# Performance work log

Hardware: AMD Instinct MI355X
Metric: run time of the kernel (lower is better)

Reference implementation:

```python
import jax, jax.numpy as jnp
import numpy as np


def setup_inputs() -> dict:
    key = jax.random.key(0)
    k1, k2, k3 = jax.random.split(key, 3)
    inp = jax.random.normal(k1, (32, 128, 56, 56), dtype=jnp.float32)
    # kaiming-style scale for a 3x3 conv kernel
    fan_in = 128 * 3 * 3
    kernel = jax.random.normal(k2, (256, 128, 3, 3), dtype=jnp.float32) * np.float32(np.sqrt(2.0 / fan_in))
    bias = jax.random.normal(k3, (256,), dtype=jnp.float32)
    return {"inp": inp, "kernel": kernel, "bias": bias}


def reference(inp, kernel, bias):
    # 3x3 conv, stride 1, padding 1 (SAME), NCHW / OIHW layout, plus bias.
    out = jax.lax.conv_general_dilated(
        inp, kernel,
        window_strides=(1, 1),
        padding=((1, 1), (1, 1)),
        dimension_numbers=("NCHW", "OIHW", "NCHW"),
    )
    return out + bias[None, :, None, None]
```

## Files before the change

### kernel.cpp

```cpp
#include <hip/hip_runtime.h>
#include <hip/hip_bf16.h>


#define C_IN   128
#define K_OUT  256
#define HW     56
#define IMG    3136
#define NBATCH 32
#define PW     58
#define IN_WS_USHORT ((size_t)4*NBATCH*PW*256*8)
#define WT_WS_USHORT ((size_t)12*2*1536*8)

typedef __bf16 bf16x8 __attribute__((ext_vector_type(8)));
typedef float  f32x4  __attribute__((ext_vector_type(4)));
typedef unsigned short ushort8 __attribute__((ext_vector_type(8)));

__device__ inline unsigned short f2bf(float f) {
    unsigned int u = __builtin_bit_cast(unsigned int, f);
    u += ((u >> 16) & 1u) + 0x7FFFu;
    return (unsigned short)(u >> 16);
}

__device__ __forceinline__ void gl2lds16(const unsigned short* g, unsigned short* l) {
    __builtin_amdgcn_global_load_lds(
        (const __attribute__((address_space(1))) unsigned int*)g,
        (__attribute__((address_space(3))) unsigned int*)l, 16, 0, 0);
}

__global__ void prep_input(const float* __restrict__ inp,
                           unsigned short* __restrict__ dst) {
    __shared__ unsigned short tile[C_IN * 57];
    int n = blockIdx.x / PW, py = blockIdx.x % PW;
    ushort8* d8 = (ushort8*)dst;
    const bool border = (py == 0 || py == PW - 1);
    if (!border) {
        const float* src = inp + (size_t)n * C_IN * IMG + (py - 1) * HW;
        for (int i = threadIdx.x; i < C_IN * HW; i += 256) {
            int c = i / HW, x = i - c * HW;
            tile[c * 57 + x] = f2bf(src[c * IMG + x]);
        }
        __syncthreads();
    }
    for (int i = threadIdx.x; i < 1024; i += 256) {
        int cq = i >> 8, rem = i & 255;
        int X = ((rem >> 6) & 3) * 16 + (rem & 15);
        int cc = (rem >> 4) & 3;
        ushort8 v = (ushort8)0;
        if (!border && X >= 1 && X <= HW) {
#pragma unroll
            for (int e = 0; e < 8; ++e)
                v[e] = tile[(cq * 32 + cc * 8 + e) * 57 + (X - 1)];
        }
        d8[((size_t)(cq * NBATCH + n) * PW + py) * 256 + rem] = v;
    }
}

__global__ void prep_weights(const float* __restrict__ w,
                             unsigned short* __restrict__ dst) {
    int chunk = blockIdx.x * 256 + threadIdx.x;
    int p = chunk / 3072, rem = chunk - p * 3072;
    int koh = rem / 1536, rem2 = rem - koh * 1536;
    int s = rem2 / 512, rem3 = rem2 - s * 512;
    int koq = rem3 >> 6, cc = (rem3 >> 4) & 3, kor = rem3 & 15;
    int ko = koh * 128 + koq * 16 + kor;
    int cq = p / 3, r = p - 3 * cq;
    ushort8 v;
#pragma unroll
    for (int e = 0; e < 8; ++e)
        v[e] = f2bf(w[(ko * C_IN + cq * 32 + cc * 8 + e) * 9 + r * 3 + s]);
    ((ushort8*)dst)[chunk] = v;
}

__global__ __launch_bounds__(128, 2) void conv_mfma(
        const unsigned short* __restrict__ In,
        const unsigned short* __restrict__ Wt,
        const float* __restrict__ bias,
        float* __restrict__ out) {
    __shared__ unsigned short smem[40960];

    const int tid = threadIdx.x;
    const int lane = tid & 63, wv = tid >> 6;
    const int l15 = lane & 15, lk = lane >> 4;
    const int koh = blockIdx.y;
    const int by = blockIdx.x;
    const int n = by / 28, rb = (by % 28) * 2;

    const int abase = wv * 4096 + lk * 256 + l15 * 16;

    int yl[7], xp[3][7];
#pragma unroll
    for (int nf = 0; nf < 7; ++nf) {
        int p = nf * 16 + l15;
        yl[nf] = p / 56;
        int x = p - yl[nf] * 56;
#pragma unroll
        for (int s = 0; s < 3; ++s) {
            int X = x + s;
            xp[s][nf] = ((X >> 4) << 10) + lk * 256 + ((X & 15) << 4);
        }
    }

    f32x4 acc[4][7];
#pragma unroll
    for (int m = 0; m < 4; ++m)
#pragma unroll
        for (int nf = 0; nf < 7; ++nf) acc[m][nf] = (f32x4)0.0f;

#define STAGE_W(P_) do {                                                    \
    const unsigned short* wg = Wt + ((size_t)((P_) * 2 + koh)) * 12288;     \
    unsigned short* wl = &smem[((P_) & 1) * 12288];                         \
    _Pragma("unroll")                                                       \
    for (int i = 0; i < 12; ++i)                                            \
        gl2lds16(wg + i * 1024 + tid * 8, wl + i * 1024 + tid * 8);         \
} while (0)

#define STAGE_ROW(C_, T_) do {                                              \
    const unsigned short* gsrc =                                            \
        In + ((size_t)(((C_) * NBATCH + n) * PW + rb + (T_))) * 2048;       \
    unsigned short* ldst = &smem[24576 + ((4 * (C_) + (T_)) & 7) * 2048];   \
    gl2lds16(gsrc + tid * 8, ldst + tid * 8);                               \
    gl2lds16(gsrc + 1024 + tid * 8, ldst + 1024 + tid * 8);                 \
} while (0)

#define STEP(PH, S_) do {                                                   \
    const char* wb = (const char*)smem + ((PH) & 1) * 24576 + (S_) * 8192;  \
    const char* ib = (const char*)smem + 49152;                             \
    bf16x8 a[4], b[7];                                                      \
    _Pragma("unroll")                                                       \
    for (int m = 0; m < 4; ++m)                                             \
        a[m] = *(const bf16x8*)(wb + abase + m * 1024);                     \
    _Pragma("unroll")                                                       \
    for (int nf = 0; nf < 7; ++nf)                                          \
        b[nf] = *(const bf16x8*)(ib + roff[nf] + xp[(S_)][nf]);             \
    __builtin_amdgcn_s_setprio(1);                                          \
    _Pragma("unroll")                                                       \
    for (int m = 0; m < 4; ++m)                                             \
        _Pragma("unroll")                                                   \
        for (int nf = 0; nf < 7; ++nf)                                      \
            acc[m][nf] = __builtin_amdgcn_mfma_f32_16x16x32_bf16(           \
                a[m], b[nf], acc[m][nf], 0, 0, 0);                          \
    __builtin_amdgcn_s_setprio(0);                                          \
} while (0)

    STAGE_W(0);
    STAGE_ROW(0, 0); STAGE_ROW(0, 1); STAGE_ROW(0, 2); STAGE_ROW(0, 3);

#define PHASE(PH) do {                                                      \
    constexpr int cqp_ = (PH) / 3, rp_ = (PH) % 3;                          \
    asm volatile("s_waitcnt vmcnt(0)" ::: "memory");                        \
    asm volatile("s_barrier" ::: "memory");                                 \
    if constexpr ((PH) < 11) STAGE_W((PH) + 1);                             \
    if constexpr (cqp_ < 3) {                                               \
        if constexpr (rp_ == 0) { STAGE_ROW(cqp_ + 1, 0); STAGE_ROW(cqp_ + 1, 1); } \
        if constexpr (rp_ == 1) { STAGE_ROW(cqp_ + 1, 2); STAGE_ROW(cqp_ + 1, 3); } \
    }                                                                       \
    asm volatile("" ::: "memory");                                          \
    { int roff[7];                                                          \
      _Pragma("unroll")                                                     \
      for (int nf = 0; nf < 7; ++nf)                                        \
          roff[nf] = ((4 * cqp_ + rp_ + yl[nf]) & 7) << 12;                 \
      STEP(PH, 0); STEP(PH, 1); STEP(PH, 2);                                \
    }                                                                       \
} while (0)

    PHASE(0);  PHASE(1);  PHASE(2);  PHASE(3);
    PHASE(4);  PHASE(5);  PHASE(6);  PHASE(7);
    PHASE(8);  PHASE(9);  PHASE(10); PHASE(11);

#undef PHASE
#undef STEP
#undef STAGE_ROW
#undef STAGE_W

    const int sp0 = rb * 56;
#pragma unroll
    for (int m = 0; m < 4; ++m) {
        int kb = koh * 128 + wv * 64 + m * 16 + lk * 4;
        f32x4 bs = *(const f32x4*)(bias + kb);
#pragma unroll
        for (int nf = 0; nf < 7; ++nf) {
            float* ob = out + ((size_t)(n * K_OUT + kb) * IMG) + sp0 + nf * 16 + l15;
#pragma unroll
            for (int j = 0; j < 4; ++j)
                ob[(size_t)j * IMG] = acc[m][nf][j] + bs[j];
        }
    }
}

__global__ void conv_naive(const float* __restrict__ inp,
                           const float* __restrict__ ker,
                           const float* __restrict__ bias,
                           float* __restrict__ out, int total) {
    int o = blockIdx.x * blockDim.x + threadIdx.x;
    if (o >= total) return;
    int x = o % HW, y = (o / HW) % HW, ko = (o / IMG) % K_OUT, n = o / (IMG * K_OUT);
    float acc = bias[ko];
    for (int c = 0; c < C_IN; ++c)
        for (int r = 0; r < 3; ++r) {
            int iy = y + r - 1; if ((unsigned)iy >= HW) continue;
            for (int s = 0; s < 3; ++s) {
                int ix = x + s - 1; if ((unsigned)ix >= HW) continue;
                acc += inp[((n * C_IN + c) * HW + iy) * HW + ix]
                     * ker[((ko * C_IN + c) * 3 + r) * 3 + s];
            }
        }
    out[o] = acc;
}

extern "C" void kernel_launch(void* const* d_in, const int* in_sizes, int n_in,
                              void* d_out, int out_size, void* d_ws, size_t ws_size,
                              hipStream_t stream) {
    const float* inp  = (const float*)d_in[0];
    const float* ker  = (const float*)d_in[1];
    const float* bias = (const float*)d_in[2];
    float* out = (float*)d_out;

    const size_t need = (IN_WS_USHORT + WT_WS_USHORT) * 2;
    if (ws_size < need) {
        int total = NBATCH * K_OUT * IMG;
        conv_naive<<<(total + 255) / 256, 256, 0, stream>>>(inp, ker, bias, out, total);
        return;
    }

    unsigned short* inb = (unsigned short*)d_ws;
    unsigned short* wtb = inb + IN_WS_USHORT;

    prep_input<<<NBATCH * PW, 256, 0, stream>>>(inp, inb);
    prep_weights<<<144, 256, 0, stream>>>(ker, wtb);

    conv_mfma<<<dim3(896, 2), 128, 0, stream>>>(inb, wtb, bias, out);
}
```

Before: 93.90 us.

## Enlarge conv tile to 256 channels by 4 rows with 8 waves and finer pipelining

```diff
diff --git a/kernel.cpp b/kernel.cpp
--- a/kernel.cpp
+++ b/kernel.cpp
@@ -9,7 +9,7 @@
 #define NBATCH 32
 #define PW     58
 #define IN_WS_USHORT ((size_t)4*NBATCH*PW*256*8)
-#define WT_WS_USHORT ((size_t)12*2*1536*8)
+#define WT_WS_USHORT ((size_t)36*1024*8)
 
 typedef __bf16 bf16x8 __attribute__((ext_vector_type(8)));
 typedef float  f32x4  __attribute__((ext_vector_type(4)));
@@ -58,39 +58,38 @@
 __global__ void prep_weights(const float* __restrict__ w,
                              unsigned short* __restrict__ dst) {
     int chunk = blockIdx.x * 256 + threadIdx.x;
-    int p = chunk / 3072, rem = chunk - p * 3072;
-    int koh = rem / 1536, rem2 = rem - koh * 1536;
-    int s = rem2 / 512, rem3 = rem2 - s * 512;
-    int koq = rem3 >> 6, cc = (rem3 >> 4) & 3, kor = rem3 & 15;
-    int ko = koh * 128 + koq * 16 + kor;
-    int cq = p / 3, r = p - 3 * cq;
+    int p = chunk >> 10, rem = chunk & 1023;
+    int koq = rem >> 6, cc = (rem >> 4) & 3, kor = rem & 15;
+    int ko = koq * 16 + kor;
+    int cq = p / 9, rs = p % 9;
+    int c0 = cq * 32 + cc * 8;
     ushort8 v;
 #pragma unroll
     for (int e = 0; e < 8; ++e)
-        v[e] = f2bf(w[(ko * C_IN + cq * 32 + cc * 8 + e) * 9 + r * 3 + s]);
+        v[e] = f2bf(w[(ko * C_IN + c0 + e) * 9 + rs]);
     ((ushort8*)dst)[chunk] = v;
 }
 
-__global__ __launch_bounds__(128, 2) void conv_mfma(
+__global__ __launch_bounds__(512, 2) void conv_mfma(
         const unsigned short* __restrict__ In,
         const unsigned short* __restrict__ Wt,
         const float* __restrict__ bias,
         float* __restrict__ out) {
-    __shared__ unsigned short smem[40960];
+    __shared__ unsigned short smem[57344];
 
     const int tid = threadIdx.x;
     const int lane = tid & 63, wv = tid >> 6;
     const int l15 = lane & 15, lk = lane >> 4;
-    const int koh = blockIdx.y;
+    const int wr = wv >> 1, wc = wv & 1;
     const int by = blockIdx.x;
-    const int n = by / 28, rb = (by % 28) * 2;
-
-    const int abase = wv * 4096 + lk * 256 + l15 * 16;
+    const int n = by / 14, rb = (by % 14) * 4;
+
+    const int albase = wr * 4096 + lk * 256 + l15 * 16;
 
     int yl[7], xp[3][7];
 #pragma unroll
     for (int nf = 0; nf < 7; ++nf) {
-        int p = nf * 16 + l15;
+        int p = wc * 112 + nf * 16 + l15;
         yl[nf] = p / 56;
         int x = p - yl[nf] * 56;
 #pragma unroll
@@ -107,31 +106,42 @@
         for (int nf = 0; nf < 7; ++nf) acc[m][nf] = (f32x4)0.0f;
 
 #define STAGE_W(P_) do {                                                    \
-    const unsigned short* wg = Wt + ((size_t)((P_) * 2 + koh)) * 12288;     \
-    unsigned short* wl = &smem[((P_) & 1) * 12288];                         \
-    _Pragma("unroll")                                                       \
-    for (int i = 0; i < 12; ++i)                                            \
-        gl2lds16(wg + i * 1024 + tid * 8, wl + i * 1024 + tid * 8);         \
+    const unsigned short* wg = Wt + (size_t)(P_) * 8192 + tid * 8;          \
+    unsigned short* wl = &smem[((P_) & 3) * 8192 + tid * 8];                \
+    gl2lds16(wg, wl);                                                       \
+    gl2lds16(wg + 4096, wl + 4096);                                         \
 } while (0)
 
-#define STAGE_ROW(C_, T_) do {                                              \
+#define STAGE_ROWS2(CQ_, T_) do {                                           \
+    int t_ = (T_) + (wv >> 2);                                              \
+    int slot_ = (6 * (CQ_) + t_) % 12;                                      \
     const unsigned short* gsrc =                                            \
-        In + ((size_t)(((C_) * NBATCH + n) * PW + rb + (T_))) * 2048;       \
-    unsigned short* ldst = &smem[24576 + ((4 * (C_) + (T_)) & 7) * 2048];   \
-    gl2lds16(gsrc + tid * 8, ldst + tid * 8);                               \
-    gl2lds16(gsrc + 1024 + tid * 8, ldst + 1024 + tid * 8);                 \
+        In + ((size_t)(((CQ_) * NBATCH + n) * PW + rb + t_)) * 2048         \
+           + (wv & 3) * 512 + lane * 8;                                     \
+    unsigned short* ldst = &smem[32768 + slot_ * 2048 + (wv & 3) * 512 + lane * 8]; \
+    gl2lds16(gsrc, ldst);                                                   \
 } while (0)
 
-#define STEP(PH, S_) do {                                                   \
-    const char* wb = (const char*)smem + ((PH) & 1) * 24576 + (S_) * 8192;  \
-    const char* ib = (const char*)smem + 49152;                             \
+#define SUBPHASE(P) do {                                                    \
+    constexpr int cq_ = (P) / 9, r_ = ((P) % 9) / 3, s_ = (P) % 3;          \
     bf16x8 a[4], b[7];                                                      \
-    _Pragma("unroll")                                                       \
-    for (int m = 0; m < 4; ++m)                                             \
-        a[m] = *(const bf16x8*)(wb + abase + m * 1024);                     \
-    _Pragma("unroll")                                                       \
-    for (int nf = 0; nf < 7; ++nf)                                          \
-        b[nf] = *(const bf16x8*)(ib + roff[nf] + xp[(S_)][nf]);             \
+    { const char* wbp = (const char*)smem + ((P) & 3) * 16384;              \
+      _Pragma("unroll")                                                     \
+      for (int m = 0; m < 4; ++m)                                           \
+          a[m] = *(const bf16x8*)(wbp + albase + m * 1024);                 \
+      const char* ibp = (const char*)smem + 65536;                          \
+      _Pragma("unroll")                                                     \
+      for (int nf = 0; nf < 7; ++nf) {                                      \
+          int t = 6 * cq_ + r_ + yl[nf]; if (t >= 12) t -= 12;              \
+          b[nf] = *(const bf16x8*)(ibp + (t << 12) + xp[s_][nf]);           \
+      }                                                                     \
+    }                                                                       \
+    if constexpr ((P) + 2 <= 35) STAGE_W((P) + 2);                          \
+    if constexpr (r_ == 0 && cq_ < 3) STAGE_ROWS2(cq_ + 1, 2 * s_);         \
+    { constexpr int cP = (((P) + 2 <= 35) ? 2 : 0)                          \
+                       + ((r_ == 0 && cq_ < 3) ? 1 : 0);                    \
+      asm volatile("s_waitcnt vmcnt(%0)" :: "i"(cP) : "memory"); }          \
+    asm volatile("s_barrier" ::: "memory");                                 \
     __builtin_amdgcn_s_setprio(1);                                          \
     _Pragma("unroll")                                                       \
     for (int m = 0; m < 4; ++m)                                             \
@@ -140,42 +150,32 @@
             acc[m][nf] = __builtin_amdgcn_mfma_f32_16x16x32_bf16(           \
                 a[m], b[nf], acc[m][nf], 0, 0, 0);                          \
     __builtin_amdgcn_s_setprio(0);                                          \
+    asm volatile("s_barrier" ::: "memory");                                 \
 } while (0)
 
-    STAGE_W(0);
-    STAGE_ROW(0, 0); STAGE_ROW(0, 1); STAGE_ROW(0, 2); STAGE_ROW(0, 3);
-
-#define PHASE(PH) do {                                                      \
-    constexpr int cqp_ = (PH) / 3, rp_ = (PH) % 3;                          \
-    asm volatile("s_waitcnt vmcnt(0)" ::: "memory");                        \
-    asm volatile("s_barrier" ::: "memory");                                 \
-    if constexpr ((PH) < 11) STAGE_W((PH) + 1);                             \
-    if constexpr (cqp_ < 3) {                                               \
-        if constexpr (rp_ == 0) { STAGE_ROW(cqp_ + 1, 0); STAGE_ROW(cqp_ + 1, 1); } \
-        if constexpr (rp_ == 1) { STAGE_ROW(cqp_ + 1, 2); STAGE_ROW(cqp_ + 1, 3); } \
-    }                                                                       \
-    asm volatile("" ::: "memory");                                          \
-    { int roff[7];                                                          \
-      _Pragma("unroll")                                                     \
-      for (int nf = 0; nf < 7; ++nf)                                        \
-          roff[nf] = ((4 * cqp_ + rp_ + yl[nf]) & 7) << 12;                 \
-      STEP(PH, 0); STEP(PH, 1); STEP(PH, 2);                                \
-    }                                                                       \
-} while (0)
-
-    PHASE(0);  PHASE(1);  PHASE(2);  PHASE(3);
-    PHASE(4);  PHASE(5);  PHASE(6);  PHASE(7);
-    PHASE(8);  PHASE(9);  PHASE(10); PHASE(11);
-
-#undef PHASE
-#undef STEP
-#undef STAGE_ROW
+    STAGE_ROWS2(0, 0); STAGE_ROWS2(0, 2); STAGE_ROWS2(0, 4);
+    STAGE_W(0); STAGE_W(1);
+    asm volatile("s_waitcnt vmcnt(2)" ::: "memory");
+    asm volatile("s_barrier" ::: "memory");
+
+    SUBPHASE(0);  SUBPHASE(1);  SUBPHASE(2);  SUBPHASE(3);
+    SUBPHASE(4);  SUBPHASE(5);  SUBPHASE(6);  SUBPHASE(7);
+    SUBPHASE(8);  SUBPHASE(9);  SUBPHASE(10); SUBPHASE(11);
+    SUBPHASE(12); SUBPHASE(13); SUBPHASE(14); SUBPHASE(15);
+    SUBPHASE(16); SUBPHASE(17); SUBPHASE(18); SUBPHASE(19);
+    SUBPHASE(20); SUBPHASE(21); SUBPHASE(22); SUBPHASE(23);
+    SUBPHASE(24); SUBPHASE(25); SUBPHASE(26); SUBPHASE(27);
+    SUBPHASE(28); SUBPHASE(29); SUBPHASE(30); SUBPHASE(31);
+    SUBPHASE(32); SUBPHASE(33); SUBPHASE(34); SUBPHASE(35);
+
+#undef SUBPHASE
+#undef STAGE_ROWS2
 #undef STAGE_W
 
-    const int sp0 = rb * 56;
+    const int sp0 = rb * 56 + wc * 112;
 #pragma unroll
     for (int m = 0; m < 4; ++m) {
-        int kb = koh * 128 + wv * 64 + m * 16 + lk * 4;
+        int kb = wr * 64 + m * 16 + lk * 4;
         f32x4 bs = *(const f32x4*)(bias + kb);
 #pragma unroll
         for (int nf = 0; nf < 7; ++nf) {
@@ -228,5 +228,5 @@
     prep_input<<<NBATCH * PW, 256, 0, stream>>>(inp, inb);
     prep_weights<<<144, 256, 0, stream>>>(ker, wtb);
 
-    conv_mfma<<<dim3(896, 2), 128, 0, stream>>>(inb, wtb, bias, out);
-}
+    conv_mfma<<<448, 512, 0, stream>>>(inb, wtb, bias, out);
+}
```

New measurement: 85.48 us. -9.0%, faster.
